# Kernel tuning notes

Hardware: AMD Instinct MI355X
Metric: run time of the kernel (lower is better)

The kernel has to match this reference:

```python
import jax, jax.numpy as jnp
import numpy as np

N = 100000  # nodes
E = 600000  # edges (avg degree ~6, mesh-like)
HID = 128


def _lin(key, fan_in, fan_out):
    # torch Linear default init: U(-1/sqrt(fan_in), 1/sqrt(fan_in))
    bound = 1.0 / np.sqrt(fan_in)
    return jax.random.uniform(key, (fan_in, fan_out), jnp.float32, -bound, bound)


def setup_inputs() -> dict:
    key = jax.random.key(0)
    ks = jax.random.split(key, 8)
    x = jax.random.normal(ks[0], (N, 3), jnp.float32)
    edge_index = jax.random.randint(ks[1], (2, E), 0, N, dtype=jnp.int32)
    return {
        "x": x,
        "edge_index": edge_index,
        "W1": _lin(ks[2], 3, HID),          "b1": jnp.zeros((HID,), jnp.float32),
        "W2": _lin(ks[3], HID, HID),        "b2": jnp.zeros((HID,), jnp.float32),
        "W3": _lin(ks[4], HID, HID // 2),   "b3": jnp.zeros((HID // 2,), jnp.float32),
        "W4": _lin(ks[5], HID // 2, HID // 2), "b4": jnp.zeros((HID // 2,), jnp.float32),
        "W5": _lin(ks[6], HID // 2, 1),     "b5": jnp.zeros((1,), jnp.float32),
    }


def reference(x, edge_index, W1, b1, W2, b2, W3, b3, W4, b4, W5, b5):
    n = x.shape[0]
    # add self loops (same graph used by every layer)
    loops = jnp.arange(n, dtype=edge_index.dtype)
    row = jnp.concatenate([edge_index[0], loops])  # sources (x_j index)
    col = jnp.concatenate([edge_index[1], loops])  # targets (aggregation index)
    # symmetric degree normalization: norm_e = d[row]^-0.5 * d[col]^-0.5
    deg = jax.ops.segment_sum(jnp.ones(col.shape, x.dtype), col, num_segments=n)
    dis = jnp.where(deg > 0, deg ** -0.5, 0.0)
    norm = (dis[row] * dis[col])[:, None]  # [E+N, 1]

    def conv(h, W, b):
        h = h @ W                                   # [N, out]
        msg = norm * h[row]                         # gather + scale  [E+N, out]
        return jax.ops.segment_sum(msg, col, num_segments=n) + b  # scatter-add

    h = jax.nn.relu(conv(x, W1, b1))
    h = jax.nn.relu(conv(h, W2, b2))
    h = jax.nn.relu(conv(h, W3, b3))
    h = jax.nn.relu(conv(h, W4, b4))
    return conv(h, W5, b5)  # [N, 1]
```

## Files before the change

### kernel.cpp

```cpp
#include <hip/hip_runtime.h>
#include <hip/hip_bf16.h>
#include <stdint.h>


#define NB 256
#define CAP 64

typedef __attribute__((ext_vector_type(8))) short bf16x8;
typedef __attribute__((ext_vector_type(4))) float f32x4;

static __host__ __device__ inline int ceil_div(int a, int b) { return (a + b - 1) / b; }

__device__ inline ushort f32_to_bf16(float x) {
    uint32_t u = __float_as_uint(x);
    uint32_t r = (u + 0x7fffu + ((u >> 16) & 1u)) >> 16;
    return (ushort)r;
}
__device__ inline float bf16_lo(uint32_t u) { return __uint_as_float(u << 16); }
__device__ inline float bf16_hi(uint32_t u) { return __uint_as_float(u & 0xffff0000u); }

__device__ inline int pad16(int deg) {
    int dp = (deg + 8) & ~7;
    return dp < 16 ? 16 : dp;
}


template <int K, int F>
__device__ inline void pack_one(const float* __restrict__ W, ushort* __restrict__ Wp, int id) {
    constexpr int KS = K / 32;
    int j = id & 7;
    int lane = (id >> 3) & 63;
    int ts = id >> 9;
    int s = ts % KS;
    int t = ts / KS;
    int k = s * 32 + ((lane >> 4) << 3) + j;
    int f = t * 16 + (lane & 15);
    Wp[id] = f32_to_bf16(W[k * F + f]);
}

__global__ void k_init(int* __restrict__ cursor, int n, int zero_blocks,
                       const float* __restrict__ W2, const float* __restrict__ W3,
                       const float* __restrict__ W4, ushort* __restrict__ Wp2,
                       ushort* __restrict__ Wp3, ushort* __restrict__ Wp4) {
    int b = blockIdx.x;
    if (b < zero_blocks) {
        int i = b * NB + threadIdx.x;
        if (i < n) cursor[i] = 0;
    } else {
        int id = (b - zero_blocks) * NB + threadIdx.x;
        if (id < 16384) pack_one<128, 128>(W2, Wp2, id);
        else if (id < 24576) pack_one<128, 64>(W3, Wp3, id - 16384);
        else if (id < 28672) pack_one<64, 64>(W4, Wp4, id - 24576);
    }
}


__global__ void k_fillb(const int* __restrict__ row, const int* __restrict__ col, int e,
                        int* __restrict__ cursor, int* __restrict__ bucket) {
    int T = (e + 7) >> 3;
    int t = blockIdx.x * NB + threadIdx.x;
    int i[8];
#pragma unroll
    for (int k = 0; k < 8; ++k) i[k] = t + k * T;
    if (i[7] < e) {
        int c[8], r[8], s[8];
#pragma unroll
        for (int k = 0; k < 8; ++k) { c[k] = col[i[k]]; r[k] = row[i[k]]; }
#pragma unroll
        for (int k = 0; k < 8; ++k) s[k] = atomicAdd(&cursor[c[k]], 1);
#pragma unroll
        for (int k = 0; k < 8; ++k) bucket[(size_t)c[k] * CAP + s[k]] = r[k];
    } else {
#pragma unroll
        for (int k = 0; k < 8; ++k) {
            if (i[k] < e) {
                int c = col[i[k]], r = row[i[k]];
                int s = atomicAdd(&cursor[c], 1);
                bucket[(size_t)c * CAP + s] = r;
            }
        }
    }
}

__global__ void k_dis(const int* __restrict__ cnt, const float* __restrict__ x,
                      float* __restrict__ dis, float4* __restrict__ xs4,
                      int* __restrict__ bucket, ushort* __restrict__ A,
                      ushort* __restrict__ B, ushort* __restrict__ C,
                      float* __restrict__ zbuf, int n) {
    int i = blockIdx.x * NB + threadIdx.x;
    if (i < n) {
        int deg = cnt[i];
        float d = rsqrtf((float)(deg + 1));
        dis[i] = d;
        xs4[i] = make_float4(d * x[3 * i], d * x[3 * i + 1], d * x[3 * i + 2], 0.f);
        int* bk = bucket + (size_t)i * CAP;
        bk[deg] = i;
        int dp = pad16(deg);
        for (int e = deg + 1; e < dp; ++e) bk[e] = n;
    } else if (i == n) {
        xs4[n] = make_float4(0.f, 0.f, 0.f, 0.f);
        zbuf[n] = 0.f;
        uint4 z = make_uint4(0, 0, 0, 0);
        uint4* Bn = (uint4*)(B + (size_t)n * 128);
        uint4* An = (uint4*)(A + (size_t)n * 64);
        uint4* Cn = (uint4*)(C + (size_t)n * 64);
#pragma unroll
        for (int k = 0; k < 16; ++k) Bn[k] = z;
#pragma unroll
        for (int k = 0; k < 8; ++k) { An[k] = z; Cn[k] = z; }
    }
}


__global__ __launch_bounds__(256) void k_l1mm(const float4* __restrict__ xs4,
                                              const int* __restrict__ cnt,
                                              const int* __restrict__ bucket,
                                              const float* __restrict__ dis,
                                              const float* __restrict__ W1,
                                              const float* __restrict__ b1,
                                              const ushort* __restrict__ Wp2,
                                              ushort* __restrict__ Zout, int n) {
    __shared__ float w[512];
    __shared__ float s_a[64][4];
    __shared__ ushort tileH[64][136];
    for (int t = threadIdx.x; t < 512; t += 256)
        w[t] = (t < 384) ? W1[t] : b1[t - 384];

    int node0 = blockIdx.x * 64;
    int local = threadIdx.x >> 2;
    int sub = threadIdx.x & 3;
    int i = node0 + local;
    float a0 = 0.f, a1 = 0.f, a2 = 0.f;
    if (i < n) {
        const int* bk = bucket + (size_t)i * CAP;
        int j0 = bk[sub], j1 = bk[sub + 4], j2 = bk[sub + 8], j3 = bk[sub + 12];
        float4 v0 = xs4[j0], v1 = xs4[j1], v2 = xs4[j2], v3 = xs4[j3];
        a0 = v0.x + v1.x + v2.x + v3.x;
        a1 = v0.y + v1.y + v2.y + v3.y;
        a2 = v0.z + v1.z + v2.z + v3.z;
        int dp = pad16(cnt[i]);
        for (int e = 16 + sub; e < dp; e += 4) {
            float4 v = xs4[bk[e]];
            a0 += v.x; a1 += v.y; a2 += v.z;
        }
    }
    a0 += __shfl_xor(a0, 1, 64); a1 += __shfl_xor(a1, 1, 64); a2 += __shfl_xor(a2, 1, 64);
    a0 += __shfl_xor(a0, 2, 64); a1 += __shfl_xor(a1, 2, 64); a2 += __shfl_xor(a2, 2, 64);
    if (sub == 0) {
        float d = (i < n) ? dis[i] : 0.f;
        s_a[local][0] = a0 * d;
        s_a[local][1] = a1 * d;
        s_a[local][2] = a2 * d;
    }
    __syncthreads();

#pragma unroll
    for (int it = 0; it < 16; ++it) {
        int id = it * 256 + threadIdx.x;
        int lc = id >> 6;
        int f = (id & 63) * 2;
        float h0 = s_a[lc][0], h1 = s_a[lc][1], h2 = s_a[lc][2];
        float v0 = fmaxf(h0 * w[f] + h1 * w[128 + f] + h2 * w[256 + f] + w[384 + f], 0.f);
        float v1 = fmaxf(h0 * w[f + 1] + h1 * w[128 + f + 1] + h2 * w[256 + f + 1] + w[384 + f + 1], 0.f);
        *(uint32_t*)&tileH[lc][f] = ((uint32_t)f32_to_bf16(v1) << 16) | (uint32_t)f32_to_bf16(v0);
    }
    __syncthreads();

    constexpr int KS = 4, FT = 8;
    int wid = threadIdx.x >> 6;
    int lane = threadIdx.x & 63;
    int m = lane & 15;
    int quad = lane >> 4;
    int tbase = wid * 16;
    bf16x8 a[KS];
#pragma unroll
    for (int s = 0; s < KS; ++s)
        a[s] = *(const bf16x8*)&tileH[tbase + m][s * 32 + quad * 8];
    float dsc[4];
#pragma unroll
    for (int r = 0; r < 4; ++r) {
        int node = node0 + tbase + quad * 4 + r;
        dsc[r] = (node < n) ? dis[node] : 0.f;
    }
    const bf16x8* bp = (const bf16x8*)Wp2;
#pragma unroll
    for (int t = 0; t < FT; ++t) {
        f32x4 acc = {0.f, 0.f, 0.f, 0.f};
#pragma unroll
        for (int s = 0; s < KS; ++s)
            acc = __builtin_amdgcn_mfma_f32_16x16x32_bf16(a[s], bp[(t * KS + s) * 64 + lane], acc, 0, 0, 0);
        int feat = t * 16 + m;
#pragma unroll
        for (int r = 0; r < 4; ++r) {
            int node = node0 + tbase + quad * 4 + r;
            if (node < n) Zout[(size_t)node * 128 + feat] = f32_to_bf16(acc[r] * dsc[r]);
        }
    }
}


__device__ inline void add8(float (&a)[8], uint4 v) {
    a[0] += bf16_lo(v.x);
    a[1] += bf16_hi(v.x);
    a[2] += bf16_lo(v.y);
    a[3] += bf16_hi(v.y);
    a[4] += bf16_lo(v.z);
    a[5] += bf16_hi(v.z);
    a[6] += bf16_lo(v.w);
    a[7] += bf16_hi(v.w);
}

template <int L>
__device__ inline void agg_sum(float (&a)[8], const uint4* __restrict__ Zq,
                               const int* __restrict__ bk, int dp, int l) {
    int4 i0 = *(const int4*)bk;
    int4 i1 = *(const int4*)(bk + 4);
    int4 i2 = *(const int4*)(bk + 8);
    int4 i3 = *(const int4*)(bk + 12);
    uint4 v0  = Zq[(size_t)i0.x * L + l];
    uint4 v1  = Zq[(size_t)i0.y * L + l];
    uint4 v2  = Zq[(size_t)i0.z * L + l];
    uint4 v3  = Zq[(size_t)i0.w * L + l];
    uint4 v4  = Zq[(size_t)i1.x * L + l];
    uint4 v5  = Zq[(size_t)i1.y * L + l];
    uint4 v6  = Zq[(size_t)i1.z * L + l];
    uint4 v7  = Zq[(size_t)i1.w * L + l];
    uint4 v8  = Zq[(size_t)i2.x * L + l];
    uint4 v9  = Zq[(size_t)i2.y * L + l];
    uint4 v10 = Zq[(size_t)i2.z * L + l];
    uint4 v11 = Zq[(size_t)i2.w * L + l];
    uint4 v12 = Zq[(size_t)i3.x * L + l];
    uint4 v13 = Zq[(size_t)i3.y * L + l];
    uint4 v14 = Zq[(size_t)i3.z * L + l];
    uint4 v15 = Zq[(size_t)i3.w * L + l];
    add8(a, v0);  add8(a, v1);  add8(a, v2);  add8(a, v3);
    add8(a, v4);  add8(a, v5);  add8(a, v6);  add8(a, v7);
    add8(a, v8);  add8(a, v9);  add8(a, v10); add8(a, v11);
    add8(a, v12); add8(a, v13); add8(a, v14); add8(a, v15);
    for (int e = 16; e < dp; e += 4) {
        int4 j4 = *(const int4*)(bk + e);
        uint4 w0 = Zq[(size_t)j4.x * L + l];
        uint4 w1 = Zq[(size_t)j4.y * L + l];
        uint4 w2 = Zq[(size_t)j4.z * L + l];
        uint4 w3 = Zq[(size_t)j4.w * L + l];
        add8(a, w0);
        add8(a, w1);
        add8(a, w2);
        add8(a, w3);
    }
}

__device__ inline uint4 pack8s(const float (&a)[8], float d, const float* __restrict__ bias, int l) {
    float4 b0 = *(const float4*)&bias[8 * l];
    float4 b1 = *(const float4*)&bias[8 * l + 4];
    float r0 = fmaxf(a[0] * d + b0.x, 0.f), r1 = fmaxf(a[1] * d + b0.y, 0.f);
    float r2 = fmaxf(a[2] * d + b0.z, 0.f), r3 = fmaxf(a[3] * d + b0.w, 0.f);
    float r4 = fmaxf(a[4] * d + b1.x, 0.f), r5 = fmaxf(a[5] * d + b1.y, 0.f);
    float r6 = fmaxf(a[6] * d + b1.z, 0.f), r7 = fmaxf(a[7] * d + b1.w, 0.f);
    uint4 o;
    o.x = ((uint32_t)f32_to_bf16(r1) << 16) | (uint32_t)f32_to_bf16(r0);
    o.y = ((uint32_t)f32_to_bf16(r3) << 16) | (uint32_t)f32_to_bf16(r2);
    o.z = ((uint32_t)f32_to_bf16(r5) << 16) | (uint32_t)f32_to_bf16(r4);
    o.w = ((uint32_t)f32_to_bf16(r7) << 16) | (uint32_t)f32_to_bf16(r6);
    return o;
}


template <int FIN, int FOUT>
__global__ __launch_bounds__(256) void k_aggmm(const ushort* __restrict__ Zin,
                                               const float* __restrict__ bias,
                                               const int* __restrict__ cnt,
                                               const int* __restrict__ bucket,
                                               const float* __restrict__ dis,
                                               const ushort* __restrict__ Wp,
                                               ushort* __restrict__ Zout, int n) {
    constexpr int L = FIN / 8;
    constexpr int GROUPS = 256 / L;
    constexpr int PASSES = 64 / GROUPS;
    __shared__ ushort tileA[64][FIN + 8];
    int node0 = blockIdx.x * 64;

    {
        int l = threadIdx.x & (L - 1);
        int g = threadIdx.x / L;
#pragma unroll
        for (int pass = 0; pass < PASSES; ++pass) {
            int local = pass * GROUPS + g;
            int i = node0 + local;
            if (i < n) {
                float a[8] = {0.f, 0.f, 0.f, 0.f, 0.f, 0.f, 0.f, 0.f};
                int dp = pad16(cnt[i]);
                agg_sum<L>(a, (const uint4*)Zin, bucket + (size_t)i * CAP, dp, l);
                *(uint4*)&tileA[local][l * 8] = pack8s(a, dis[i], bias, l);
            }
        }
    }
    __syncthreads();

    constexpr int KS = FIN / 32;
    constexpr int FT = FOUT / 16;
    int wid = threadIdx.x >> 6;
    int lane = threadIdx.x & 63;
    int m = lane & 15;
    int quad = lane >> 4;
    int tbase = wid * 16;
    bf16x8 a[KS];
#pragma unroll
    for (int s = 0; s < KS; ++s)
        a[s] = *(const bf16x8*)&tileA[tbase + m][s * 32 + quad * 8];
    float dsc[4];
#pragma unroll
    for (int r = 0; r < 4; ++r) {
        int node = node0 + tbase + quad * 4 + r;
        dsc[r] = (node < n) ? dis[node] : 0.f;
    }
    const bf16x8* bp = (const bf16x8*)Wp;
#pragma unroll
    for (int t = 0; t < FT; ++t) {
        f32x4 acc = {0.f, 0.f, 0.f, 0.f};
#pragma unroll
        for (int s = 0; s < KS; ++s)
            acc = __builtin_amdgcn_mfma_f32_16x16x32_bf16(a[s], bp[(t * KS + s) * 64 + lane], acc, 0, 0, 0);
        int feat = t * 16 + m;
#pragma unroll
        for (int r = 0; r < 4; ++r) {
            int node = node0 + tbase + quad * 4 + r;
            if (node < n) Zout[(size_t)node * FOUT + feat] = f32_to_bf16(acc[r] * dsc[r]);
        }
    }
}

__global__ __launch_bounds__(256) void k_agg64z(const ushort* __restrict__ Z,
                                                const float* __restrict__ bias,
                                                const float* __restrict__ W5,
                                                const int* __restrict__ cnt,
                                                const int* __restrict__ bucket,
                                                const float* __restrict__ dis,
                                                float* __restrict__ zbuf, int n) {
    int l = threadIdx.x & 7;
    int i = blockIdx.x * 32 + (threadIdx.x >> 3);
    if (i >= n) return;
    float a[8] = {0.f, 0.f, 0.f, 0.f, 0.f, 0.f, 0.f, 0.f};
    int dp = pad16(cnt[i]);
    agg_sum<8>(a, (const uint4*)Z, bucket + (size_t)i * CAP, dp, l);
    float d = dis[i];
    float4 b0 = *(const float4*)&bias[8 * l];
    float4 b1 = *(const float4*)&bias[8 * l + 4];
    float4 w0 = *(const float4*)&W5[8 * l];
    float4 w1 = *(const float4*)&W5[8 * l + 4];
    float p = fmaxf(a[0] * d + b0.x, 0.f) * w0.x + fmaxf(a[1] * d + b0.y, 0.f) * w0.y +
              fmaxf(a[2] * d + b0.z, 0.f) * w0.z + fmaxf(a[3] * d + b0.w, 0.f) * w0.w +
              fmaxf(a[4] * d + b1.x, 0.f) * w1.x + fmaxf(a[5] * d + b1.y, 0.f) * w1.y +
              fmaxf(a[6] * d + b1.z, 0.f) * w1.z + fmaxf(a[7] * d + b1.w, 0.f) * w1.w;
#pragma unroll
    for (int off = 4; off; off >>= 1) p += __shfl_xor(p, off, 64);
    if (l == 0) zbuf[i] = d * p;
}

__global__ void k_agg1(const float* __restrict__ zbuf, const float* __restrict__ b5,
                       const int* __restrict__ cnt, const int* __restrict__ bucket,
                       const float* __restrict__ dis, float* __restrict__ out, int n) {
    int i = blockIdx.x * NB + threadIdx.x;
    if (i >= n) return;
    const int* bk = bucket + (size_t)i * CAP;
    int4 i0 = *(const int4*)bk;
    int4 i1 = *(const int4*)(bk + 4);
    int4 i2 = *(const int4*)(bk + 8);
    int4 i3 = *(const int4*)(bk + 12);
    float acc = zbuf[i0.x] + zbuf[i0.y] + zbuf[i0.z] + zbuf[i0.w] +
                zbuf[i1.x] + zbuf[i1.y] + zbuf[i1.z] + zbuf[i1.w] +
                zbuf[i2.x] + zbuf[i2.y] + zbuf[i2.z] + zbuf[i2.w] +
                zbuf[i3.x] + zbuf[i3.y] + zbuf[i3.z] + zbuf[i3.w];
    int dp = pad16(cnt[i]);
    for (int e = 16; e < dp; e += 4) {
        int4 j4 = *(const int4*)(bk + e);
        acc += zbuf[j4.x] + zbuf[j4.y] + zbuf[j4.z] + zbuf[j4.w];
    }
    out[i] = dis[i] * acc + b5[0];
}


static inline size_t align_up(size_t x) { return (x + 255) & ~(size_t)255; }

extern "C" void kernel_launch(void* const* d_in, const int* in_sizes, int n_in,
                              void* d_out, int out_size, void* d_ws, size_t ws_size,
                              hipStream_t stream) {
    const int n = in_sizes[0] / 3;
    const int e = in_sizes[1] / 2;

    const float* x   = (const float*)d_in[0];
    const int*   ei  = (const int*)d_in[1];
    const int*   row = ei;
    const int*   col = ei + e;
    const float* W1 = (const float*)d_in[2];  const float* b1 = (const float*)d_in[3];
    const float* W2 = (const float*)d_in[4];  const float* b2 = (const float*)d_in[5];
    const float* W3 = (const float*)d_in[6];  const float* b3 = (const float*)d_in[7];
    const float* W4 = (const float*)d_in[8];  const float* b4 = (const float*)d_in[9];
    const float* W5 = (const float*)d_in[10]; const float* b5 = (const float*)d_in[11];
    float* out = (float*)d_out;

    char* base = (char*)d_ws;
    size_t off = 0;
    auto alloc = [&](size_t bytes) { char* p = base + off; off = align_up(off + bytes); return p; };
    int*    cursor = (int*)alloc((size_t)n * 4);
    float*  dis    = (float*)alloc((size_t)n * 4);
    float4* xs4    = (float4*)alloc((size_t)(n + 1) * 16);
    int*    bucket = (int*)alloc((size_t)n * CAP * 4);
    ushort* A      = (ushort*)alloc((size_t)(n + 1) * 64 * 2);
    ushort* B      = (ushort*)alloc((size_t)(n + 1) * 128 * 2);
    ushort* C      = (ushort*)alloc((size_t)(n + 1) * 64 * 2);
    float*  zbuf   = (float*)alloc((size_t)(n + 1) * 4);
    ushort* Wp2    = (ushort*)alloc(128 * 128 * 2);
    ushort* Wp3    = (ushort*)alloc(128 * 64 * 2);
    ushort* Wp4    = (ushort*)alloc(64 * 64 * 2);
    (void)ws_size;

    const int gn = ceil_div(n, NB);
    const int pack_blocks = ceil_div(16384 + 8192 + 4096, NB);

    k_init<<<gn + pack_blocks, NB, 0, stream>>>(cursor, n, gn, W2, W3, W4, Wp2, Wp3, Wp4);
    k_fillb<<<ceil_div(ceil_div(e, 8), NB), NB, 0, stream>>>(row, col, e, cursor, bucket);
    k_dis<<<gn, NB, 0, stream>>>(cursor, x, dis, xs4, bucket, A, B, C, zbuf, n);

    k_l1mm<<<ceil_div(n, 64), 256, 0, stream>>>(xs4, cursor, bucket, dis, W1, b1, Wp2, B, n);

    k_aggmm<128, 64><<<ceil_div(n, 64), 256, 0, stream>>>(B, b2, cursor, bucket, dis, Wp3, A, n);

    k_aggmm<64, 64><<<ceil_div(n, 64), 256, 0, stream>>>(A, b3, cursor, bucket, dis, Wp4, C, n);

    k_agg64z<<<ceil_div(n, 32), 256, 0, stream>>>(C, b4, W5, cursor, bucket, dis, zbuf, n);

    k_agg1<<<gn, NB, 0, stream>>>(zbuf, b5, cursor, bucket, dis, out, n);
}
```

Measured before the change: 219.4 us.

## Gather neighbor rows via async global-to-LDS loads in aggregation kernels

Replaces the per-thread register gather of the first 16 padded neighbor rows with global_load_lds async copies into shared memory, then sums from LDS, in the layer 2/3/4 aggregation kernels. The 128-input and 64-input aggregation-matmul kernels are specialized and use smaller node tiles (16 and 32 nodes per block) with the MFMA work redistributed across waves. The aim is more memory-level parallelism and higher occupancy for the latency-bound gather. In exchange it adds LDS footprint and a full vmcnt wait, and it relies on padding entries pointing to the zero row n.

Measured after the change: 244.1 us. 11.3% more time.

```diff
diff --git a/kernel.cpp b/kernel.cpp
--- a/kernel.cpp
+++ b/kernel.cpp
@@ -22,6 +22,12 @@
 __device__ inline int pad16(int deg) {
     int dp = (deg + 8) & ~7;
     return dp < 16 ? 16 : dp;
+}
+
+__device__ inline void async_row16(const void* src, void* lds_base) {
+    __builtin_amdgcn_global_load_lds(
+        (const __attribute__((address_space(1))) void*)src,
+        (__attribute__((address_space(3))) void*)lds_base, 16, 0, 0);
 }
 
 
@@ -210,46 +216,6 @@
     a[7] += bf16_hi(v.w);
 }
 
-template <int L>
-__device__ inline void agg_sum(float (&a)[8], const uint4* __restrict__ Zq,
-                               const int* __restrict__ bk, int dp, int l) {
-    int4 i0 = *(const int4*)bk;
-    int4 i1 = *(const int4*)(bk + 4);
-    int4 i2 = *(const int4*)(bk + 8);
-    int4 i3 = *(const int4*)(bk + 12);
-    uint4 v0  = Zq[(size_t)i0.x * L + l];
-    uint4 v1  = Zq[(size_t)i0.y * L + l];
-    uint4 v2  = Zq[(size_t)i0.z * L + l];
-    uint4 v3  = Zq[(size_t)i0.w * L + l];
-    uint4 v4  = Zq[(size_t)i1.x * L + l];
-    uint4 v5  = Zq[(size_t)i1.y * L + l];
-    uint4 v6  = Zq[(size_t)i1.z * L + l];
-    uint4 v7  = Zq[(size_t)i1.w * L + l];
-    uint4 v8  = Zq[(size_t)i2.x * L + l];
-    uint4 v9  = Zq[(size_t)i2.y * L + l];
-    uint4 v10 = Zq[(size_t)i2.z * L + l];
-    uint4 v11 = Zq[(size_t)i2.w * L + l];
-    uint4 v12 = Zq[(size_t)i3.x * L + l];
-    uint4 v13 = Zq[(size_t)i3.y * L + l];
-    uint4 v14 = Zq[(size_t)i3.z * L + l];
-    uint4 v15 = Zq[(size_t)i3.w * L + l];
-    add8(a, v0);  add8(a, v1);  add8(a, v2);  add8(a, v3);
-    add8(a, v4);  add8(a, v5);  add8(a, v6);  add8(a, v7);
-    add8(a, v8);  add8(a, v9);  add8(a, v10); add8(a, v11);
-    add8(a, v12); add8(a, v13); add8(a, v14); add8(a, v15);
-    for (int e = 16; e < dp; e += 4) {
-        int4 j4 = *(const int4*)(bk + e);
-        uint4 w0 = Zq[(size_t)j4.x * L + l];
-        uint4 w1 = Zq[(size_t)j4.y * L + l];
-        uint4 w2 = Zq[(size_t)j4.z * L + l];
-        uint4 w3 = Zq[(size_t)j4.w * L + l];
-        add8(a, w0);
-        add8(a, w1);
-        add8(a, w2);
-        add8(a, w3);
-    }
-}
-
 __device__ inline uint4 pack8s(const float (&a)[8], float d, const float* __restrict__ bias, int l) {
     float4 b0 = *(const float4*)&bias[8 * l];
     float4 b1 = *(const float4*)&bias[8 * l + 4];
@@ -266,48 +232,134 @@
 }
 
 
-template <int FIN, int FOUT>
-__global__ __launch_bounds__(256) void k_aggmm(const ushort* __restrict__ Zin,
-                                               const float* __restrict__ bias,
-                                               const int* __restrict__ cnt,
-                                               const int* __restrict__ bucket,
-                                               const float* __restrict__ dis,
-                                               const ushort* __restrict__ Wp,
-                                               ushort* __restrict__ Zout, int n) {
-    constexpr int L = FIN / 8;
-    constexpr int GROUPS = 256 / L;
-    constexpr int PASSES = 64 / GROUPS;
-    __shared__ ushort tileA[64][FIN + 8];
-    int node0 = blockIdx.x * 64;
-
-    {
-        int l = threadIdx.x & (L - 1);
-        int g = threadIdx.x / L;
-#pragma unroll
-        for (int pass = 0; pass < PASSES; ++pass) {
-            int local = pass * GROUPS + g;
-            int i = node0 + local;
-            if (i < n) {
-                float a[8] = {0.f, 0.f, 0.f, 0.f, 0.f, 0.f, 0.f, 0.f};
-                int dp = pad16(cnt[i]);
-                agg_sum<L>(a, (const uint4*)Zin, bucket + (size_t)i * CAP, dp, l);
-                *(uint4*)&tileA[local][l * 8] = pack8s(a, dis[i], bias, l);
-            }
-        }
-    }
-    __syncthreads();
-
-    constexpr int KS = FIN / 32;
-    constexpr int FT = FOUT / 16;
+__global__ __launch_bounds__(256) void k_aggmm128(const ushort* __restrict__ Zin,
+                                                  const float* __restrict__ bias,
+                                                  const int* __restrict__ cnt,
+                                                  const int* __restrict__ bucket,
+                                                  const float* __restrict__ dis,
+                                                  const ushort* __restrict__ Wp,
+                                                  ushort* __restrict__ Zout, int n) {
+    __shared__ uint4 S[16][16][16];
+    __shared__ ushort tile[16][136];
+    int node0 = blockIdx.x * 16;
     int wid = threadIdx.x >> 6;
     int lane = threadIdx.x & 63;
+    int l16 = lane & 15;
+    int gnode = node0 + wid * 4 + (lane >> 4);
+    int idxv = (gnode < n) ? bucket[(size_t)gnode * CAP + l16] : n;
+#pragma unroll
+    for (int k = 0; k < 16; ++k) {
+        int idx = __shfl(idxv, (lane & 48) | k, 64);
+        async_row16(Zin + (size_t)idx * 128 + l16 * 8, &S[k][wid * 4][0]);
+    }
+    asm volatile("s_waitcnt vmcnt(0)" ::: "memory");
+    __builtin_amdgcn_sched_barrier(0);
+
+    int g = threadIdx.x >> 4;
+    int l = threadIdx.x & 15;
+    int i = node0 + g;
+    float a[8] = {0.f, 0.f, 0.f, 0.f, 0.f, 0.f, 0.f, 0.f};
+#pragma unroll
+    for (int s = 0; s < 16; ++s) add8(a, S[s][g][l]);
+    if (i < n) {
+        int dp = pad16(cnt[i]);
+        if (dp > 16) {
+            const int* bk = bucket + (size_t)i * CAP;
+            const uint4* Zq = (const uint4*)Zin;
+            for (int e = 16; e < dp; e += 4) {
+                int4 j4 = *(const int4*)(bk + e);
+                add8(a, Zq[(size_t)j4.x * 16 + l]);
+                add8(a, Zq[(size_t)j4.y * 16 + l]);
+                add8(a, Zq[(size_t)j4.z * 16 + l]);
+                add8(a, Zq[(size_t)j4.w * 16 + l]);
+            }
+        }
+        *(uint4*)&tile[g][l * 8] = pack8s(a, dis[i], bias, l);
+    }
+    __syncthreads();
+
     int m = lane & 15;
     int quad = lane >> 4;
-    int tbase = wid * 16;
-    bf16x8 a[KS];
-#pragma unroll
-    for (int s = 0; s < KS; ++s)
-        a[s] = *(const bf16x8*)&tileA[tbase + m][s * 32 + quad * 8];
+    bf16x8 af[4];
+#pragma unroll
+    for (int s = 0; s < 4; ++s)
+        af[s] = *(const bf16x8*)&tile[m][s * 32 + quad * 8];
+    float dsc[4];
+#pragma unroll
+    for (int r = 0; r < 4; ++r) {
+        int node = node0 + quad * 4 + r;
+        dsc[r] = (node < n) ? dis[node] : 0.f;
+    }
+    const bf16x8* bp = (const bf16x8*)Wp;
+    int t = wid;
+    f32x4 acc = {0.f, 0.f, 0.f, 0.f};
+#pragma unroll
+    for (int s = 0; s < 4; ++s)
+        acc = __builtin_amdgcn_mfma_f32_16x16x32_bf16(af[s], bp[(t * 4 + s) * 64 + lane], acc, 0, 0, 0);
+    int feat = t * 16 + m;
+#pragma unroll
+    for (int r = 0; r < 4; ++r) {
+        int node = node0 + quad * 4 + r;
+        if (node < n) Zout[(size_t)node * 64 + feat] = f32_to_bf16(acc[r] * dsc[r]);
+    }
+}
+
+
+__global__ __launch_bounds__(256) void k_aggmm64(const ushort* __restrict__ Zin,
+                                                 const float* __restrict__ bias,
+                                                 const int* __restrict__ cnt,
+                                                 const int* __restrict__ bucket,
+                                                 const float* __restrict__ dis,
+                                                 const ushort* __restrict__ Wp,
+                                                 ushort* __restrict__ Zout, int n) {
+    __shared__ uint4 S[16][32][8];
+    __shared__ ushort tile[32][72];
+    int node0 = blockIdx.x * 32;
+    int wid = threadIdx.x >> 6;
+    int lane = threadIdx.x & 63;
+    int l8 = lane & 7;
+    int gnode = node0 + wid * 8 + (lane >> 3);
+    int idxA = (gnode < n) ? bucket[(size_t)gnode * CAP + l8] : n;
+    int idxB = (gnode < n) ? bucket[(size_t)gnode * CAP + 8 + l8] : n;
+#pragma unroll
+    for (int k = 0; k < 16; ++k) {
+        int sel = (k < 8) ? idxA : idxB;
+        int idx = __shfl(sel, (lane & 56) | (k & 7), 64);
+        async_row16(Zin + (size_t)idx * 64 + l8 * 8, &S[k][wid * 8][0]);
+    }
+    asm volatile("s_waitcnt vmcnt(0)" ::: "memory");
+    __builtin_amdgcn_sched_barrier(0);
+
+    int g = threadIdx.x >> 3;
+    int l = threadIdx.x & 7;
+    int i = node0 + g;
+    float a[8] = {0.f, 0.f, 0.f, 0.f, 0.f, 0.f, 0.f, 0.f};
+#pragma unroll
+    for (int s = 0; s < 16; ++s) add8(a, S[s][g][l]);
+    if (i < n) {
+        int dp = pad16(cnt[i]);
+        if (dp > 16) {
+            const int* bk = bucket + (size_t)i * CAP;
+            const uint4* Zq = (const uint4*)Zin;
+            for (int e = 16; e < dp; e += 4) {
+                int4 j4 = *(const int4*)(bk + e);
+                add8(a, Zq[(size_t)j4.x * 8 + l]);
+                add8(a, Zq[(size_t)j4.y * 8 + l]);
+                add8(a, Zq[(size_t)j4.z * 8 + l]);
+                add8(a, Zq[(size_t)j4.w * 8 + l]);
+            }
+        }
+        *(uint4*)&tile[g][l * 8] = pack8s(a, dis[i], bias, l);
+    }
+    __syncthreads();
+
+    int m = lane & 15;
+    int quad = lane >> 4;
+    int tbase = (wid & 1) * 16;
+    bf16x8 af[2];
+#pragma unroll
+    for (int s = 0; s < 2; ++s)
+        af[s] = *(const bf16x8*)&tile[tbase + m][s * 32 + quad * 8];
     float dsc[4];
 #pragma unroll
     for (int r = 0; r < 4; ++r) {
@@ -316,19 +368,21 @@
     }
     const bf16x8* bp = (const bf16x8*)Wp;
 #pragma unroll
-    for (int t = 0; t < FT; ++t) {
+    for (int tt = 0; tt < 2; ++tt) {
+        int t = (wid >> 1) * 2 + tt;
         f32x4 acc = {0.f, 0.f, 0.f, 0.f};
 #pragma unroll
-        for (int s = 0; s < KS; ++s)
-            acc = __builtin_amdgcn_mfma_f32_16x16x32_bf16(a[s], bp[(t * KS + s) * 64 + lane], acc, 0, 0, 0);
+        for (int s = 0; s < 2; ++s)
+            acc = __builtin_amdgcn_mfma_f32_16x16x32_bf16(af[s], bp[(t * 2 + s) * 64 + lane], acc, 0, 0, 0);
         int feat = t * 16 + m;
 #pragma unroll
         for (int r = 0; r < 4; ++r) {
             int node = node0 + tbase + quad * 4 + r;
-            if (node < n) Zout[(size_t)node * FOUT + feat] = f32_to_bf16(acc[r] * dsc[r]);
-        }
-    }
-}
+            if (node < n) Zout[(size_t)node * 64 + feat] = f32_to_bf16(acc[r] * dsc[r]);
+        }
+    }
+}
+
 
 __global__ __launch_bounds__(256) void k_agg64z(const ushort* __restrict__ Z,
                                                 const float* __restrict__ bias,
@@ -337,12 +391,42 @@
                                                 const int* __restrict__ bucket,
                                                 const float* __restrict__ dis,
                                                 float* __restrict__ zbuf, int n) {
+    __shared__ uint4 S[16][32][8];
+    int node0 = blockIdx.x * 32;
+    int wid = threadIdx.x >> 6;
+    int lane = threadIdx.x & 63;
+    int l8 = lane & 7;
+    int gnode = node0 + wid * 8 + (lane >> 3);
+    int idxA = (gnode < n) ? bucket[(size_t)gnode * CAP + l8] : n;
+    int idxB = (gnode < n) ? bucket[(size_t)gnode * CAP + 8 + l8] : n;
+#pragma unroll
+    for (int k = 0; k < 16; ++k) {
+        int sel = (k < 8) ? idxA : idxB;
+        int idx = __shfl(sel, (lane & 56) | (k & 7), 64);
+        async_row16(Z + (size_t)idx * 64 + l8 * 8, &S[k][wid * 8][0]);
+    }
+    asm volatile("s_waitcnt vmcnt(0)" ::: "memory");
+    __builtin_amdgcn_sched_barrier(0);
+
+    int g = threadIdx.x >> 3;
     int l = threadIdx.x & 7;
-    int i = blockIdx.x * 32 + (threadIdx.x >> 3);
+    int i = node0 + g;
     if (i >= n) return;
     float a[8] = {0.f, 0.f, 0.f, 0.f, 0.f, 0.f, 0.f, 0.f};
+#pragma unroll
+    for (int s = 0; s < 16; ++s) add8(a, S[s][g][l]);
     int dp = pad16(cnt[i]);
-    agg_sum<8>(a, (const uint4*)Z, bucket + (size_t)i * CAP, dp, l);
+    if (dp > 16) {
+        const int* bk = bucket + (size_t)i * CAP;
+        const uint4* Zq = (const uint4*)Z;
+        for (int e = 16; e < dp; e += 4) {
+            int4 j4 = *(const int4*)(bk + e);
+            add8(a, Zq[(size_t)j4.x * 8 + l]);
+            add8(a, Zq[(size_t)j4.y * 8 + l]);
+            add8(a, Zq[(size_t)j4.z * 8 + l]);
+            add8(a, Zq[(size_t)j4.w * 8 + l]);
+        }
+    }
     float d = dis[i];
     float4 b0 = *(const float4*)&bias[8 * l];
     float4 b1 = *(const float4*)&bias[8 * l + 4];
@@ -424,9 +508,9 @@
 
     k_l1mm<<<ceil_div(n, 64), 256, 0, stream>>>(xs4, cursor, bucket, dis, W1, b1, Wp2, B, n);
 
-    k_aggmm<128, 64><<<ceil_div(n, 64), 256, 0, stream>>>(B, b2, cursor, bucket, dis, Wp3, A, n);
-
-    k_aggmm<64, 64><<<ceil_div(n, 64), 256, 0, stream>>>(A, b3, cursor, bucket, dis, Wp4, C, n);
+    k_aggmm128<<<ceil_div(n, 16), 256, 0, stream>>>(B, b2, cursor, bucket, dis, Wp3, A, n);
+
+    k_aggmm64<<<ceil_div(n, 32), 256, 0, stream>>>(A, b3, cursor, bucket, dis, Wp4, C, n);
 
     k_agg64z<<<ceil_div(n, 32), 256, 0, stream>>>(C, b4, W5, cursor, bucket, dis, zbuf, n);
 
```
